# Kernel optimization log

Measured on AMD Instinct MI355X. Metric: run time of the kernel, lower is better.

The kernel has to match this reference:

```python
import jax, jax.numpy as jnp
import numpy as np

N_LEAVES = 32768
DEPTH = 16               # tree levels, leaves at level 0
N_NODES = 2 * N_LEAVES - 1
H = 256                  # h_size
X = 300                  # x_size
FEAT = 1024              # image feature_size
R = 49                   # image regions
VOCAB = 30000
CLASSES = 5


def setup_inputs() -> dict:
    ks = jax.random.split(jax.random.key(0), 10)
    wordid = jax.random.randint(ks[0], (N_NODES,), 0, VOCAB, dtype=jnp.int32)
    # leaves carry word tokens (mask=1), internal nodes don't (mask=0)
    mask = jnp.concatenate([jnp.ones(N_LEAVES, jnp.int32),
                            jnp.zeros(N_NODES - N_LEAVES, jnp.int32)])
    image = jax.random.normal(ks[1], (R, FEAT), dtype=jnp.float32)
    h0 = jnp.zeros((N_NODES, H), jnp.float32)
    c0 = jnp.zeros((N_NODES, H), jnp.float32)
    s = lambda k, shp, fan: jax.random.normal(k, shp, dtype=jnp.float32) * (1.0 / np.sqrt(fan))
    emb = s(ks[2], (VOCAB, X), X)
    attn_w_in = s(ks[3], (X, FEAT), FEAT)            # Attention.linear_in (no bias)
    attn_w_out = s(ks[4], (X, X + FEAT), X + FEAT)   # Attention.linear_out
    attn_b_out = jnp.zeros((X,), jnp.float32)
    w_iou = s(ks[5], (3 * H, X), X)                  # cell.W_iou (no bias)
    u_iou = s(ks[6], (3 * H, 2 * H), 2 * H)          # cell.U_iou (no bias)
    b_iou = jnp.zeros((1, 3 * H), jnp.float32)
    u_f_w = s(ks[7], (2 * H, 2 * H), 2 * H)          # cell.U_f
    u_f_b = jnp.zeros((2 * H,), jnp.float32)
    lin_w = s(ks[8], (CLASSES, H), H)                # final classifier
    lin_b = jnp.zeros((CLASSES,), jnp.float32)
    return dict(wordid=wordid, mask=mask, image=image, h0=h0, c0=c0, emb=emb,
                attn_w_in=attn_w_in, attn_w_out=attn_w_out, attn_b_out=attn_b_out,
                w_iou=w_iou, u_iou=u_iou, b_iou=b_iou, u_f_w=u_f_w, u_f_b=u_f_b,
                lin_w=lin_w, lin_b=lin_b)


def _forward(wordid, mask, image, h0, c0, emb, attn_w_in, attn_w_out, attn_b_out,
             w_iou, u_iou, b_iou, u_f_w, u_f_b, lin_w, lin_b):
    # --- embedding + attention over image regions ---
    embeds = emb[wordid * mask]                                  # [N, X]
    img_in = image @ attn_w_in.T                                 # [R, X]
    atten = jax.nn.softmax(embeds @ img_in.T, axis=1)            # [N, R]
    context = atten @ image                                      # [N, FEAT]
    sent = jnp.tanh(jnp.concatenate([context, embeds], axis=1) @ attn_w_out.T + attn_b_out)
    iou_x = (sent @ w_iou.T) * mask[:, None].astype(sent.dtype)  # [N, 3H] (dropout p=0 -> identity)

    def apply_node(iou, c_in):
        i, o, u = jnp.split(iou + b_iou, 3, axis=1)
        c_new = jax.nn.sigmoid(i) * jnp.tanh(u) + c_in
        return jax.nn.sigmoid(o) * jnp.tanh(c_new), c_new

    # --- leaves: no mailbox, apply_node with initial c ---
    h_leaf, c_leaf = apply_node(iou_x[:N_LEAVES], c0[:N_LEAVES])
    h = h0.at[:N_LEAVES].set(h_leaf)
    c = c0.at[:N_LEAVES].set(c_leaf)

    # --- topological propagation, one dense level at a time ---
    off_prev, sz, off = 0, N_LEAVES, N_LEAVES
    for _ in range(DEPTH - 1):
        sz_new = sz // 2
        h_cat = jax.lax.dynamic_slice_in_dim(h, off_prev, sz).reshape(sz_new, 2 * H)
        c_ch = jax.lax.dynamic_slice_in_dim(c, off_prev, sz).reshape(sz_new, 2, H)
        f = jax.nn.sigmoid(h_cat @ u_f_w.T + u_f_b).reshape(sz_new, 2, H)
        c_red = jnp.sum(f * c_ch, axis=1)                        # [sz_new, H]
        iou = h_cat @ u_iou.T                                    # reduce_func overwrites node iou
        h_new, c_new = apply_node(iou, c_red)
        h = h.at[off:off + sz_new].set(h_new)
        c = c.at[off:off + sz_new].set(c_new)
        off_prev, sz, off = off, sz_new, off + sz_new

    return h @ lin_w.T + lin_b                                   # [N, CLASSES]


def reference(wordid, mask, image, h0, c0, emb, attn_w_in, attn_w_out, attn_b_out,
              w_iou, u_iou, b_iou, u_f_w, u_f_b, lin_w, lin_b):
    return _forward(wordid, mask, image, h0, c0, emb, attn_w_in, attn_w_out, attn_b_out,
                    w_iou, u_iou, b_iou, u_f_w, u_f_b, lin_w, lin_b)
```

## Files before the change

kernel.cpp:

```cpp
#include <hip/hip_runtime.h>
#include <hip/hip_bf16.h>
#include <math.h>

#define N_LEAVES 32768
#define N_NODES  65535
#define DEPTH    16
#define H        256
#define XS       300
#define FEAT     1024
#define RR       49
#define CLASSES  5

#define XP 320
#define CATW 384

typedef __attribute__((ext_vector_type(8))) short bf16x8;
typedef __attribute__((ext_vector_type(4))) float f32x4;

__device__ __forceinline__ ushort f2bf(float v) {
    __hip_bfloat16 h = __float2bfloat16(v);
    return *reinterpret_cast<ushort*>(&h);
}
__device__ __forceinline__ float bf2f(ushort u) {
    __hip_bfloat16 h; *reinterpret_cast<ushort*>(&h) = u;
    return __bfloat162float(h);
}

__device__ __forceinline__ float fsig(float x) {
    float e = __builtin_amdgcn_exp2f(-1.44269504f * x);
    return __builtin_amdgcn_rcpf(1.0f + e);
}
__device__ __forceinline__ float ftanh(float x) {
    float xx = fmaxf(x, -20.0f);
    float e = __builtin_amdgcn_exp2f(-2.88539008f * xx);
    return (1.0f - e) * __builtin_amdgcn_rcpf(1.0f + e);
}
__device__ __forceinline__ float fexp(float x) {
    return __builtin_amdgcn_exp2f(1.44269504f * x);
}

#define SPIN() __builtin_amdgcn_sched_barrier(0)
#define SBAR() { __builtin_amdgcn_s_barrier(); __builtin_amdgcn_sched_barrier(0); }

__device__ __forceinline__ void swz_mj(int& mblk, int& jg) {
    int lid = blockIdx.y * gridDim.x + blockIdx.x;
    int mcount = gridDim.y, njg = gridDim.x;
    if ((mcount & 7) == 0) {
        int xcd = lid & 7, q = lid >> 3;
        jg = q % njg;
        mblk = xcd * (mcount >> 3) + q / njg;
    } else { mblk = blockIdx.y; jg = blockIdx.x; }
}

__device__ __forceinline__ ushort* lds_at(ushort* base, int row, int kbyte) {
    int off = row * 128 + kbyte;
    off ^= ((row & 7) << 4);
    return (ushort*)((char*)base + off);
}

__device__ __forceinline__ void gll16(const void* g, void* l) {
    __builtin_amdgcn_global_load_lds(
        (const __attribute__((address_space(1))) unsigned int*)g,
        (__attribute__((address_space(3))) unsigned int*)l, 16, 0, 0);
}

__device__ __forceinline__ void issue_tileA(const ushort* A, long lda, long m0, long mmax,
                                            int k0, ushort* buf, int R, int w, int lane)
{
    const int insts = R >> 5;
#pragma unroll
    for (int q = 0; q < 4; ++q) {
        if (q >= insts) break;
        int dest = (w * insts + q) * 1024;
        int row = (dest >> 7) + (lane >> 3);
        int kb = ((lane & 7) << 4) ^ ((row & 7) << 4);
        long am = m0 + row; if (am > mmax) am = mmax;
        gll16((const char*)(A + am * lda + k0) + kb, (char*)buf + dest);
    }
}

__global__ __launch_bounds__(256)
void k_sent(const ushort* __restrict__ A, const ushort* __restrict__ Wf,
            const float* __restrict__ bias, ushort* __restrict__ Cbf)
{
    __shared__ ushort At[3][128 * 64];
    const int tid = threadIdx.x;
    const int l = tid & 63;
    const int w = tid >> 6;
    int mblk, nb; swz_mj(mblk, nb);
    const long m0 = (long)mblk * 128;
    const ushort* wb = Wf + (size_t)(nb * 4 + w) * 24 * 512 + l * 8;

    bf16x8 wreg[2][2][2];
    f32x4 acc[2][8] = {};

    auto loadW = [&](int t, int buf) {
        const ushort* wt = wb + (long)t * 4 * 512;
#pragma unroll
        for (int kk = 0; kk < 2; ++kk)
#pragma unroll
            for (int j = 0; j < 2; ++j)
                wreg[buf][kk][j] = *(const bf16x8*)(wt + (long)(kk * 2 + j) * 512);
    };

    issue_tileA(A, CATW, m0, N_LEAVES - 1, 0, At[0], 128, w, l);
    __syncthreads();
    issue_tileA(A, CATW, m0, N_LEAVES - 1, 64, At[1], 128, w, l);
    SPIN();
    loadW(0, 0);
#pragma unroll
    for (int t = 0; t < 6; ++t) {
        if (t + 2 < 6) issue_tileA(A, CATW, m0, N_LEAVES - 1, (t + 2) * 64, At[(t + 2) % 3], 128, w, l);
        SPIN();
        if (t + 1 < 6) loadW(t + 1, (t + 1) & 1);
        ushort* Ab = At[t % 3];
#pragma unroll
        for (int kk = 0; kk < 2; ++kk) {
            bf16x8 af[8];
#pragma unroll
            for (int i = 0; i < 8; ++i)
                af[i] = *(const bf16x8*)lds_at(Ab, i * 16 + (l & 15), kk * 64 + (l >> 4) * 16);
#pragma unroll
            for (int j = 0; j < 2; ++j)
#pragma unroll
                for (int i = 0; i < 8; ++i)
                    acc[j][i] = __builtin_amdgcn_mfma_f32_16x16x32_bf16(af[i], wreg[t & 1][kk][j], acc[j][i], 0, 0, 0);
        }
        if (t + 1 < 6) SBAR();
    }
#pragma unroll
    for (int j = 0; j < 2; ++j) {
        long n = (long)nb * 128 + w * 32 + j * 16 + (l & 15);
        if (n >= XS) continue;
        float bn = bias[n];
#pragma unroll
        for (int i = 0; i < 8; ++i)
#pragma unroll
            for (int r = 0; r < 4; ++r) {
                long m = m0 + i * 16 + (l >> 4) * 4 + r;
                Cbf[m * XP + n] = f2bf(ftanh(acc[j][i][r] + bn));
            }
    }
}

__global__ __launch_bounds__(256)
void k_attn(const float* __restrict__ emb, const int* __restrict__ wid,
            const ushort* __restrict__ img, ushort* __restrict__ cat)
{
    __shared__ ushort At[128 * 64];
    __shared__ ushort Bt[64 * 64];
    const int tid = threadIdx.x;
    const int l = tid & 63;
    const int w = tid >> 6;
    const long m0 = (long)blockIdx.x * 128;
    const int srow = tid >> 3, skg = tid & 7;

    int wrd[4];
#pragma unroll
    for (int q = 0; q < 4; ++q) wrd[q] = wid[m0 + q * 32 + srow];

    float av[4][8];
    bf16x8 breg[2];
    f32x4 acc[2][4] = {};

    auto loadAB = [&](int t) {
        int c = t * 64 + skg * 8;
#pragma unroll
        for (int q = 0; q < 4; ++q) {
            const float* er = emb + (long)wrd[q] * XS;
            if (c + 8 <= XS) {
                float4 a = *(const float4*)(er + c);
                float4 b = *(const float4*)(er + c + 4);
                av[q][0] = a.x; av[q][1] = a.y; av[q][2] = a.z; av[q][3] = a.w;
                av[q][4] = b.x; av[q][5] = b.y; av[q][6] = b.z; av[q][7] = b.w;
            } else {
#pragma unroll
                for (int u = 0; u < 8; ++u) av[q][u] = (c + u < XS) ? er[c + u] : 0.f;
            }
        }
#pragma unroll
        for (int q = 0; q < 2; ++q)
            breg[q] = *(const bf16x8*)(img + (long)(q * 32 + srow) * XP + t * 64 + skg * 8);
    };
    auto writeAB = [&](int t) {
        int c = t * 64 + skg * 8;
#pragma unroll
        for (int q = 0; q < 4; ++q) {
            int row = q * 32 + srow;
            bf16x8 pk;
#pragma unroll
            for (int u = 0; u < 8; ++u) pk[u] = (short)f2bf(av[q][u]);
            *(bf16x8*)lds_at(At, row, skg * 16) = pk;
            *(bf16x8*)(cat + (m0 + row) * CATW + 64 + c) = pk;
        }
#pragma unroll
        for (int q = 0; q < 2; ++q)
            *(bf16x8*)lds_at(Bt, q * 32 + srow, skg * 16) = breg[q];
    };

    loadAB(0);
    writeAB(0);
    for (int t = 0; t < 5; ++t) {
        __syncthreads();
        if (t + 1 < 5) loadAB(t + 1);
#pragma unroll
        for (int kk = 0; kk < 2; ++kk) {
            bf16x8 af[2], bg[4];
#pragma unroll
            for (int i = 0; i < 2; ++i)
                af[i] = *(const bf16x8*)lds_at(At, w * 32 + i * 16 + (l & 15), kk * 64 + (l >> 4) * 16);
#pragma unroll
            for (int j = 0; j < 4; ++j)
                bg[j] = *(const bf16x8*)lds_at(Bt, j * 16 + (l & 15), kk * 64 + (l >> 4) * 16);
#pragma unroll
            for (int i = 0; i < 2; ++i)
#pragma unroll
                for (int j = 0; j < 4; ++j)
                    acc[i][j] = __builtin_amdgcn_mfma_f32_16x16x32_bf16(af[i], bg[j], acc[i][j], 0, 0, 0);
        }
        if (t + 1 < 5) {
            __syncthreads();
            writeAB(t + 1);
        }
    }
#pragma unroll
    for (int i = 0; i < 2; ++i)
#pragma unroll
        for (int r = 0; r < 4; ++r) {
            long m = m0 + w * 32 + i * 16 + (l >> 4) * 4 + r;
            float v[4]; float mx = -1e30f;
#pragma unroll
            for (int j = 0; j < 4; ++j) {
                int n = j * 16 + (l & 15);
                v[j] = (n < RR) ? acc[i][j][r] : -1e30f;
                mx = fmaxf(mx, v[j]);
            }
#pragma unroll
            for (int sh = 1; sh < 16; sh <<= 1) mx = fmaxf(mx, __shfl_xor(mx, sh));
            float e[4], s = 0.f;
#pragma unroll
            for (int j = 0; j < 4; ++j) { e[j] = fexp(v[j] - mx); s += e[j]; }
#pragma unroll
            for (int sh = 1; sh < 16; sh <<= 1) s += __shfl_xor(s, sh);
            float inv = __builtin_amdgcn_rcpf(s);
#pragma unroll
            for (int j = 0; j < 4; ++j)
                cat[m * CATW + j * 16 + (l & 15)] = f2bf(e[j] * inv);
        }
}

__global__ __launch_bounds__(256)
void k_leaf_fused(const ushort* __restrict__ A, const ushort* __restrict__ Wf,
                  const float* __restrict__ b_iou,
                  ushort* __restrict__ h, ushort* __restrict__ c)
{
    __shared__ ushort At[3][128 * 64];
    const int tid = threadIdx.x;
    const int l = tid & 63;
    const int w = tid >> 6;
    int mblk, jg; swz_mj(mblk, jg);
    const long m0 = (long)mblk * 128;
    const ushort* wb = Wf + (size_t)(jg * 4 + w) * 30 * 512 + l * 8;

    bf16x8 wreg[2][2][3];
    f32x4 acc[3][8] = {};

    auto loadW = [&](int t, int buf) {
        const ushort* wt = wb + (long)t * 6 * 512;
#pragma unroll
        for (int kk = 0; kk < 2; ++kk)
#pragma unroll
            for (int g = 0; g < 3; ++g)
                wreg[buf][kk][g] = *(const bf16x8*)(wt + (long)(kk * 3 + g) * 512);
    };

    issue_tileA(A, XP, m0, N_LEAVES - 1, 0, At[0], 128, w, l);
    __syncthreads();
    issue_tileA(A, XP, m0, N_LEAVES - 1, 64, At[1], 128, w, l);
    SPIN();
    loadW(0, 0);
#pragma unroll
    for (int t = 0; t < 5; ++t) {
        if (t + 2 < 5) issue_tileA(A, XP, m0, N_LEAVES - 1, (t + 2) * 64, At[(t + 2) % 3], 128, w, l);
        SPIN();
        if (t + 1 < 5) loadW(t + 1, (t + 1) & 1);
        ushort* Ab = At[t % 3];
#pragma unroll
        for (int kk = 0; kk < 2; ++kk) {
            bf16x8 af[8];
#pragma unroll
            for (int i = 0; i < 8; ++i)
                af[i] = *(const bf16x8*)lds_at(Ab, i * 16 + (l & 15), kk * 64 + (l >> 4) * 16);
#pragma unroll
            for (int g = 0; g < 3; ++g)
#pragma unroll
                for (int i = 0; i < 8; ++i)
                    acc[g][i] = __builtin_amdgcn_mfma_f32_16x16x32_bf16(af[i], wreg[t & 1][kk][g], acc[g][i], 0, 0, 0);
        }
        if (t + 1 < 5) SBAR();
    }
    {
        int jglob = jg * 64 + w * 16 + (l & 15);
        float bi = b_iou[jglob], bu = b_iou[512 + jglob], bo = b_iou[256 + jglob];
#pragma unroll
        for (int i = 0; i < 8; ++i)
#pragma unroll
            for (int r = 0; r < 4; ++r) {
                long m = m0 + i * 16 + (l >> 4) * 4 + r;
                float cn = fsig(acc[0][i][r] + bi) * ftanh(acc[1][i][r] + bu);
                c[m * H + jglob] = f2bf(cn);
                h[m * H + jglob] = f2bf(fsig(acc[2][i][r] + bo) * ftanh(cn));
            }
    }
}

__global__ __launch_bounds__(256)
void k_tree_fused(const ushort* __restrict__ A, const ushort* __restrict__ Wf,
                  const float* __restrict__ u_f_b, const float* __restrict__ b_iou,
                  const ushort* __restrict__ csrc,
                  ushort* __restrict__ hdst, ushort* __restrict__ cdst, int sz_new)
{
    __shared__ ushort At[3][64 * 64];
    const int tid = threadIdx.x;
    const int l = tid & 63;
    const int w = tid >> 6;
    int mblk, jg; swz_mj(mblk, jg);
    const long m0 = (long)mblk * 64;
    const ushort* wb = Wf + (size_t)(jg * 4 + w) * 80 * 512 + l * 8;

    bf16x8 wreg[2][2][5];
    f32x4 acc[5][4] = {};

    auto loadW = [&](int t, int buf) {
        const ushort* wt = wb + (long)t * 10 * 512;
#pragma unroll
        for (int kk = 0; kk < 2; ++kk)
#pragma unroll
            for (int g = 0; g < 5; ++g)
                wreg[buf][kk][g] = *(const bf16x8*)(wt + (long)(kk * 5 + g) * 512);
    };

    issue_tileA(A, 512, m0, sz_new - 1, 0, At[0], 64, w, l);
    __syncthreads();
    issue_tileA(A, 512, m0, sz_new - 1, 64, At[1], 64, w, l);
    SPIN();
    loadW(0, 0);
#pragma unroll
    for (int t = 0; t < 8; ++t) {
        if (t + 2 < 8) issue_tileA(A, 512, m0, sz_new - 1, (t + 2) * 64, At[(t + 2) % 3], 64, w, l);
        SPIN();
        if (t + 1 < 8) loadW(t + 1, (t + 1) & 1);
        ushort* Ab = At[t % 3];
#pragma unroll
        for (int kk = 0; kk < 2; ++kk) {
            bf16x8 af[4];
#pragma unroll
            for (int i = 0; i < 4; ++i)
                af[i] = *(const bf16x8*)lds_at(Ab, i * 16 + (l & 15), kk * 64 + (l >> 4) * 16);
#pragma unroll
            for (int g = 0; g < 5; ++g)
#pragma unroll
                for (int i = 0; i < 4; ++i)
                    acc[g][i] = __builtin_amdgcn_mfma_f32_16x16x32_bf16(af[i], wreg[t & 1][kk][g], acc[g][i], 0, 0, 0);
        }
        if (t + 1 < 8) SBAR();
    }
    {
        int jglob = jg * 64 + w * 16 + (l & 15);
        float bf0 = u_f_b[jglob], bf1 = u_f_b[256 + jglob];
        float bi = b_iou[jglob], bu = b_iou[512 + jglob], bo = b_iou[256 + jglob];
#pragma unroll
        for (int i = 0; i < 4; ++i)
#pragma unroll
            for (int r = 0; r < 4; ++r) {
                long m = m0 + i * 16 + (l >> 4) * 4 + r;
                if (m < sz_new) {
                    float cl = bf2f(csrc[(2 * m) * H + jglob]);
                    float cr = bf2f(csrc[(2 * m + 1) * H + jglob]);
                    float S = fsig(acc[0][i][r] + bf0) * cl
                            + fsig(acc[1][i][r] + bf1) * cr;
                    float cn = fsig(acc[2][i][r] + bi) * ftanh(acc[3][i][r] + bu) + S;
                    cdst[m * H + jglob] = f2bf(cn);
                    hdst[m * H + jglob] = f2bf(fsig(acc[4][i][r] + bo) * ftanh(cn));
                }
            }
    }
}

__global__ __launch_bounds__(256)
void k_prep(const float* __restrict__ image, const float* __restrict__ w_in,
            const float* __restrict__ w_out, ushort* __restrict__ img_bf,
            ushort* __restrict__ wcat)
{
    const int wave = (blockIdx.x * 256 + threadIdx.x) >> 6;
    const int lane = threadIdx.x & 63;
    const int half = RR * XS;
    if (wave >= 2 * half) return;
    const float* wr; const float* ir; ushort* outp;
    if (wave < half) {
        int r = wave / XS, x = wave % XS;
        ir = image + (long)r * FEAT;
        wr = w_in + (long)x * FEAT;
        outp = img_bf + (long)r * XP + x;
    } else {
        int w2 = wave - half;
        int x = w2 / RR, r = w2 % RR;
        ir = image + (long)r * FEAT;
        wr = w_out + (long)x * (FEAT + XS);
        outp = wcat + (long)x * CATW + r;
    }
    float s = 0.f;
#pragma unroll
    for (int u = 0; u < FEAT / 64; ++u) {
        int f = lane + u * 64;
        s = fmaf(ir[f], wr[f], s);
    }
#pragma unroll
    for (int sh = 32; sh; sh >>= 1) s += __shfl_xor(s, sh);
    if (lane == 0) *outp = f2bf(s);
}

__global__ __launch_bounds__(256)
void k_cvt(ushort* __restrict__ dst, long dld, long doff,
           const float* __restrict__ src, long sld, long soff,
           int rows, int cols)
{
    long idx = (long)blockIdx.x * 256 + threadIdx.x;
    if (idx >= (long)rows * cols) return;
    int r = (int)(idx / cols), c = (int)(idx % cols);
    dst[r * dld + doff + c] = f2bf(src[r * sld + soff + c]);
}

__global__ __launch_bounds__(256)
void k_bld_wcatf(ushort* __restrict__ dst, const ushort* __restrict__ wcat)
{
    long idx = (long)blockIdx.x * 256 + threadIdx.x;
    if (idx >= 147456) return;
    int u = idx & 7; long r = idx >> 3;
    int l = r & 63; r >>= 6;
    int j = r & 1; r >>= 1;
    int kk = r & 1; r >>= 1;
    int t = (int)(r % 6); r /= 6;
    int wq = r & 3; r >>= 2;
    int nb = (int)r;
    int row = nb * 128 + wq * 32 + j * 16 + (l & 15);
    int col = t * 64 + kk * 32 + (l >> 4) * 8 + u;
    dst[idx] = wcat[(long)row * CATW + col];
}

__global__ __launch_bounds__(256)
void k_bld_w3f(ushort* __restrict__ dst, const float* __restrict__ w_iou)
{
    long idx = (long)blockIdx.x * 256 + threadIdx.x;
    if (idx >= 245760) return;
    int u = idx & 7; long r = idx >> 3;
    int l = r & 63; r >>= 6;
    int g = (int)(r % 3); r /= 3;
    int kk = r & 1; r >>= 1;
    int t = (int)(r % 5); r /= 5;
    int wq = r & 3; r >>= 2;
    int jg = (int)r;
    int row = jg * 64 + wq * 16 + (l & 15);
    int col = t * 64 + kk * 32 + (l >> 4) * 8 + u;
    int srow = (g == 0) ? row : (g == 1) ? 512 + row : 256 + row;
    dst[idx] = (col < XS) ? f2bf(w_iou[(long)srow * XS + col]) : 0;
}

__global__ __launch_bounds__(256)
void k_bld_w5f(ushort* __restrict__ dst, const float* __restrict__ u_f_w,
               const float* __restrict__ u_iou)
{
    long idx = (long)blockIdx.x * 256 + threadIdx.x;
    if (idx >= 655360) return;
    int u = idx & 7; long r = idx >> 3;
    int l = r & 63; r >>= 6;
    int g = (int)(r % 5); r /= 5;
    int kk = r & 1; r >>= 1;
    int t = (int)(r & 7); r >>= 3;
    int wq = r & 3; r >>= 2;
    int jg = (int)r;
    int row = jg * 64 + wq * 16 + (l & 15);
    int col = t * 64 + kk * 32 + (l >> 4) * 8 + u;
    const float* src;
    if (g == 0)      src = u_f_w + (long)row * 512;
    else if (g == 1) src = u_f_w + (long)(256 + row) * 512;
    else if (g == 2) src = u_iou + (long)row * 512;
    else if (g == 3) src = u_iou + (long)(512 + row) * 512;
    else             src = u_iou + (long)(256 + row) * 512;
    dst[idx] = f2bf(src[col]);
}

__global__ __launch_bounds__(256)
void k_classify(const ushort* __restrict__ h, const float* __restrict__ lin_w,
                const float* __restrict__ lin_b, float* __restrict__ out, int n_rows)
{
    const int node = (int)((blockIdx.x * 256 + threadIdx.x) >> 6);
    const int lane = threadIdx.x & 63;
    if (node >= n_rows) return;
    const ushort* hr = h + (long)node * H;
    float p[CLASSES] = {0.f};
#pragma unroll
    for (int u = 0; u < H / 64; ++u) {
        int j = lane + u * 64;
        float hv = bf2f(hr[j]);
#pragma unroll
        for (int cc = 0; cc < CLASSES; ++cc)
            p[cc] = fmaf(hv, lin_w[cc * H + j], p[cc]);
    }
#pragma unroll
    for (int cc = 0; cc < CLASSES; ++cc)
#pragma unroll
        for (int sh = 32; sh; sh >>= 1) p[cc] += __shfl_xor(p[cc], sh);
    if (lane == 0) {
#pragma unroll
        for (int cc = 0; cc < CLASSES; ++cc)
            out[(long)node * CLASSES + cc] = p[cc] + lin_b[cc];
    }
}

extern "C" void kernel_launch(void* const* d_in, const int* in_sizes, int n_in,
                              void* d_out, int out_size, void* d_ws, size_t ws_size,
                              hipStream_t stream)
{
    const int*   wordid     = (const int*)  d_in[0];
    const float* image      = (const float*)d_in[2];
    const float* emb        = (const float*)d_in[5];
    const float* attn_w_in  = (const float*)d_in[6];
    const float* attn_w_out = (const float*)d_in[7];
    const float* attn_b_out = (const float*)d_in[8];
    const float* w_iou      = (const float*)d_in[9];
    const float* u_iou      = (const float*)d_in[10];
    const float* b_iou      = (const float*)d_in[11];
    const float* u_f_w      = (const float*)d_in[12];
    const float* u_f_b      = (const float*)d_in[13];
    const float* lin_w      = (const float*)d_in[14];
    const float* lin_b      = (const float*)d_in[15];
    float* out = (float*)d_out;

    char* p = (char*)d_ws;
    auto alloc = [&](size_t bytes) { char* r = p; p += (bytes + 255) & ~255UL; return r; };
    ushort* cat     = (ushort*)alloc((size_t)N_LEAVES * CATW * 2);
    ushort* sentbf  = (ushort*)alloc((size_t)N_LEAVES * XP * 2);
    ushort* hall    = (ushort*)alloc((size_t)65536 * H * 2);
    ushort* cA      = (ushort*)alloc((size_t)N_LEAVES * H * 2);
    ushort* cB      = (ushort*)alloc((size_t)(N_LEAVES/2) * H * 2);
    ushort* img_bf  = (ushort*)alloc((size_t)64 * XP * 2);
    ushort* wcat    = (ushort*)alloc((size_t)CATW * CATW * 2);
    ushort* wcatf   = (ushort*)alloc((size_t)147456 * 2);
    ushort* w3f     = (ushort*)alloc((size_t)245760 * 2);
    ushort* w5f     = (ushort*)alloc((size_t)655360 * 2);
    (void)ws_size;

    hipMemsetAsync(img_bf, 0, (size_t)64 * XP * 2, stream);
    hipMemsetAsync(wcat,   0, (size_t)CATW * CATW * 2, stream);
    {
        int waves = 2 * RR * XS;
        k_prep<<<(waves * 64 + 255) / 256, 256, 0, stream>>>(image, attn_w_in,
                                                             attn_w_out, img_bf, wcat);
    }
    k_cvt<<<((long)XS * XS + 255) / 256, 256, 0, stream>>>(
        wcat, CATW, 64, attn_w_out, FEAT + XS, FEAT, XS, XS);
    k_bld_wcatf<<<(147456 + 255) / 256, 256, 0, stream>>>(wcatf, wcat);
    k_bld_w3f<<<(245760 + 255) / 256, 256, 0, stream>>>(w3f, w_iou);
    k_bld_w5f<<<(655360 + 255) / 256, 256, 0, stream>>>(w5f, u_f_w, u_iou);

    k_attn<<<N_LEAVES / 128, 256, 0, stream>>>(emb, wordid, img_bf, cat);
    k_sent<<<dim3(3, N_LEAVES / 128), 256, 0, stream>>>(cat, wcatf, attn_b_out, sentbf);
    k_leaf_fused<<<dim3(4, N_LEAVES / 128), 256, 0, stream>>>(
        sentbf, w3f, b_iou, hall, cA);

    ushort* csrc = cA; ushort* cdst = cB;
    int node_off = N_LEAVES;
    int sz = N_LEAVES;
    int off_prev = 0;
    for (int lvl = 0; lvl < DEPTH - 1; ++lvl) {
        int sz_new = sz / 2;
        k_tree_fused<<<dim3(4, (sz_new + 63) / 64), 256, 0, stream>>>(
            hall + (long)off_prev * H, w5f, u_f_b, b_iou, csrc,
            hall + (long)node_off * H, cdst, sz_new);
        off_prev = node_off;
        node_off += sz_new;
        ushort* t = csrc; csrc = cdst; cdst = t;
        sz = sz_new;
    }

    k_classify<<<((long)N_NODES * 64 + 255) / 256, 256, 0, stream>>>(
        hall, lin_w, lin_b, out, N_NODES);
}
```

Before: 315.4 us.

## Deepen tree-kernel A-tile pipeline, merge prep kernels, vectorize classifier

The tree-level kernel now keeps four LDS A-tile buffers with a prefetch distance of three, and issues the next weight-register load before the wait rather than after. The four setup kernels (image projection, conversion, w3f and w5f builds) are merged into one launch that dispatches on block index, cutting launch overhead. The classifier now reads h and lin_w with vector loads. Risks include higher LDS use, which may lower occupancy, and an extra barrier per iteration in the tree kernel.

```diff
diff --git a/kernel.cpp b/kernel.cpp
--- a/kernel.cpp
+++ b/kernel.cpp
@@ -320,7 +320,7 @@
                   const ushort* __restrict__ csrc,
                   ushort* __restrict__ hdst, ushort* __restrict__ cdst, int sz_new)
 {
-    __shared__ ushort At[3][64 * 64];
+    __shared__ ushort At[4][64 * 64];
     const int tid = threadIdx.x;
     const int l = tid & 63;
     const int w = tid >> 6;
@@ -345,12 +345,15 @@
     issue_tileA(A, 512, m0, sz_new - 1, 64, At[1], 64, w, l);
     SPIN();
     loadW(0, 0);
+    SPIN();
+    issue_tileA(A, 512, m0, sz_new - 1, 128, At[2], 64, w, l);
 #pragma unroll
     for (int t = 0; t < 8; ++t) {
-        if (t + 2 < 8) issue_tileA(A, 512, m0, sz_new - 1, (t + 2) * 64, At[(t + 2) % 3], 64, w, l);
+        if (t + 1 < 8) loadW(t + 1, (t + 1) & 1);
         SPIN();
-        if (t + 1 < 8) loadW(t + 1, (t + 1) & 1);
-        ushort* Ab = At[t % 3];
+        if (t + 3 < 8) issue_tileA(A, 512, m0, sz_new - 1, (t + 3) * 64, At[(t + 3) & 3], 64, w, l);
+        SPIN();
+        ushort* Ab = At[t & 3];
 #pragma unroll
         for (int kk = 0; kk < 2; ++kk) {
             bf16x8 af[4];
@@ -387,52 +390,89 @@
     }
 }
 
-__global__ __launch_bounds__(256)
-void k_prep(const float* __restrict__ image, const float* __restrict__ w_in,
-            const float* __restrict__ w_out, ushort* __restrict__ img_bf,
-            ushort* __restrict__ wcat)
-{
-    const int wave = (blockIdx.x * 256 + threadIdx.x) >> 6;
-    const int lane = threadIdx.x & 63;
-    const int half = RR * XS;
-    if (wave >= 2 * half) return;
-    const float* wr; const float* ir; ushort* outp;
-    if (wave < half) {
-        int r = wave / XS, x = wave % XS;
-        ir = image + (long)r * FEAT;
-        wr = w_in + (long)x * FEAT;
-        outp = img_bf + (long)r * XP + x;
+#define PREP_NB   7350
+#define CVT_NB    352
+#define W3F_NB    960
+#define W5F_NB    2560
+
+__global__ __launch_bounds__(256)
+void k_prep_a(const float* __restrict__ image, const float* __restrict__ w_in,
+              const float* __restrict__ w_out, const float* __restrict__ w_iou,
+              const float* __restrict__ u_f_w, const float* __restrict__ u_iou,
+              ushort* __restrict__ img_bf, ushort* __restrict__ wcat,
+              ushort* __restrict__ w3f, ushort* __restrict__ w5f)
+{
+    int b = blockIdx.x;
+    if (b < PREP_NB) {
+        const int wave = (b * 256 + threadIdx.x) >> 6;
+        const int lane = threadIdx.x & 63;
+        const int half = RR * XS;
+        if (wave >= 2 * half) return;
+        const float* wr; const float* ir; ushort* outp;
+        if (wave < half) {
+            int r = wave / XS, x = wave % XS;
+            ir = image + (long)r * FEAT;
+            wr = w_in + (long)x * FEAT;
+            outp = img_bf + (long)r * XP + x;
+        } else {
+            int w2 = wave - half;
+            int x = w2 / RR, r = w2 % RR;
+            ir = image + (long)r * FEAT;
+            wr = w_out + (long)x * (FEAT + XS);
+            outp = wcat + (long)x * CATW + r;
+        }
+        float s = 0.f;
+#pragma unroll
+        for (int u = 0; u < FEAT / 64; ++u) {
+            int f = lane + u * 64;
+            s = fmaf(ir[f], wr[f], s);
+        }
+#pragma unroll
+        for (int sh = 32; sh; sh >>= 1) s += __shfl_xor(s, sh);
+        if (lane == 0) *outp = f2bf(s);
+    } else if (b < PREP_NB + CVT_NB) {
+        long idx = (long)(b - PREP_NB) * 256 + threadIdx.x;
+        if (idx >= (long)XS * XS) return;
+        int r = (int)(idx / XS), cc = (int)(idx % XS);
+        wcat[(long)r * CATW + 64 + cc] = f2bf(w_out[(long)r * (FEAT + XS) + FEAT + cc]);
+    } else if (b < PREP_NB + CVT_NB + W3F_NB) {
+        long idx = (long)(b - PREP_NB - CVT_NB) * 256 + threadIdx.x;
+        if (idx >= 245760) return;
+        int u = idx & 7; long r = idx >> 3;
+        int l = r & 63; r >>= 6;
+        int g = (int)(r % 3); r /= 3;
+        int kk = r & 1; r >>= 1;
+        int t = (int)(r % 5); r /= 5;
+        int wq = r & 3; r >>= 2;
+        int jg = (int)r;
+        int row = jg * 64 + wq * 16 + (l & 15);
+        int col = t * 64 + kk * 32 + (l >> 4) * 8 + u;
+        int srow = (g == 0) ? row : (g == 1) ? 512 + row : 256 + row;
+        w3f[idx] = (col < XS) ? f2bf(w_iou[(long)srow * XS + col]) : 0;
     } else {
-        int w2 = wave - half;
-        int x = w2 / RR, r = w2 % RR;
-        ir = image + (long)r * FEAT;
-        wr = w_out + (long)x * (FEAT + XS);
-        outp = wcat + (long)x * CATW + r;
-    }
-    float s = 0.f;
-#pragma unroll
-    for (int u = 0; u < FEAT / 64; ++u) {
-        int f = lane + u * 64;
-        s = fmaf(ir[f], wr[f], s);
-    }
-#pragma unroll
-    for (int sh = 32; sh; sh >>= 1) s += __shfl_xor(s, sh);
-    if (lane == 0) *outp = f2bf(s);
-}
-
-__global__ __launch_bounds__(256)
-void k_cvt(ushort* __restrict__ dst, long dld, long doff,
-           const float* __restrict__ src, long sld, long soff,
-           int rows, int cols)
-{
-    long idx = (long)blockIdx.x * 256 + threadIdx.x;
-    if (idx >= (long)rows * cols) return;
-    int r = (int)(idx / cols), c = (int)(idx % cols);
-    dst[r * dld + doff + c] = f2bf(src[r * sld + soff + c]);
-}
-
-__global__ __launch_bounds__(256)
-void k_bld_wcatf(ushort* __restrict__ dst, const ushort* __restrict__ wcat)
+        long idx = (long)(b - PREP_NB - CVT_NB - W3F_NB) * 256 + threadIdx.x;
+        if (idx >= 655360) return;
+        int u = idx & 7; long r = idx >> 3;
+        int l = r & 63; r >>= 6;
+        int g = (int)(r % 5); r /= 5;
+        int kk = r & 1; r >>= 1;
+        int t = (int)(r & 7); r >>= 3;
+        int wq = r & 3; r >>= 2;
+        int jg = (int)r;
+        int row = jg * 64 + wq * 16 + (l & 15);
+        int col = t * 64 + kk * 32 + (l >> 4) * 8 + u;
+        const float* src;
+        if (g == 0)      src = u_f_w + (long)row * 512;
+        else if (g == 1) src = u_f_w + (long)(256 + row) * 512;
+        else if (g == 2) src = u_iou + (long)row * 512;
+        else if (g == 3) src = u_iou + (long)(512 + row) * 512;
+        else             src = u_iou + (long)(256 + row) * 512;
+        w5f[idx] = f2bf(src[col]);
+    }
+}
+
+__global__ __launch_bounds__(256)
+void k_prep_b(ushort* __restrict__ dst, const ushort* __restrict__ wcat)
 {
     long idx = (long)blockIdx.x * 256 + threadIdx.x;
     if (idx >= 147456) return;
@@ -449,63 +489,19 @@
 }
 
 __global__ __launch_bounds__(256)
-void k_bld_w3f(ushort* __restrict__ dst, const float* __restrict__ w_iou)
-{
-    long idx = (long)blockIdx.x * 256 + threadIdx.x;
-    if (idx >= 245760) return;
-    int u = idx & 7; long r = idx >> 3;
-    int l = r & 63; r >>= 6;
-    int g = (int)(r % 3); r /= 3;
-    int kk = r & 1; r >>= 1;
-    int t = (int)(r % 5); r /= 5;
-    int wq = r & 3; r >>= 2;
-    int jg = (int)r;
-    int row = jg * 64 + wq * 16 + (l & 15);
-    int col = t * 64 + kk * 32 + (l >> 4) * 8 + u;
-    int srow = (g == 0) ? row : (g == 1) ? 512 + row : 256 + row;
-    dst[idx] = (col < XS) ? f2bf(w_iou[(long)srow * XS + col]) : 0;
-}
-
-__global__ __launch_bounds__(256)
-void k_bld_w5f(ushort* __restrict__ dst, const float* __restrict__ u_f_w,
-               const float* __restrict__ u_iou)
-{
-    long idx = (long)blockIdx.x * 256 + threadIdx.x;
-    if (idx >= 655360) return;
-    int u = idx & 7; long r = idx >> 3;
-    int l = r & 63; r >>= 6;
-    int g = (int)(r % 5); r /= 5;
-    int kk = r & 1; r >>= 1;
-    int t = (int)(r & 7); r >>= 3;
-    int wq = r & 3; r >>= 2;
-    int jg = (int)r;
-    int row = jg * 64 + wq * 16 + (l & 15);
-    int col = t * 64 + kk * 32 + (l >> 4) * 8 + u;
-    const float* src;
-    if (g == 0)      src = u_f_w + (long)row * 512;
-    else if (g == 1) src = u_f_w + (long)(256 + row) * 512;
-    else if (g == 2) src = u_iou + (long)row * 512;
-    else if (g == 3) src = u_iou + (long)(512 + row) * 512;
-    else             src = u_iou + (long)(256 + row) * 512;
-    dst[idx] = f2bf(src[col]);
-}
-
-__global__ __launch_bounds__(256)
 void k_classify(const ushort* __restrict__ h, const float* __restrict__ lin_w,
                 const float* __restrict__ lin_b, float* __restrict__ out, int n_rows)
 {
     const int node = (int)((blockIdx.x * 256 + threadIdx.x) >> 6);
     const int lane = threadIdx.x & 63;
     if (node >= n_rows) return;
-    const ushort* hr = h + (long)node * H;
-    float p[CLASSES] = {0.f};
-#pragma unroll
-    for (int u = 0; u < H / 64; ++u) {
-        int j = lane + u * 64;
-        float hv = bf2f(hr[j]);
-#pragma unroll
-        for (int cc = 0; cc < CLASSES; ++cc)
-            p[cc] = fmaf(hv, lin_w[cc * H + j], p[cc]);
+    ushort4 hv4 = *(const ushort4*)(h + (long)node * H + lane * 4);
+    float hv[4] = { bf2f(hv4.x), bf2f(hv4.y), bf2f(hv4.z), bf2f(hv4.w) };
+    float p[CLASSES];
+#pragma unroll
+    for (int cc = 0; cc < CLASSES; ++cc) {
+        float4 wv = *(const float4*)(lin_w + (long)cc * H + lane * 4);
+        p[cc] = hv[0] * wv.x + hv[1] * wv.y + hv[2] * wv.z + hv[3] * wv.w;
     }
 #pragma unroll
     for (int cc = 0; cc < CLASSES; ++cc)
@@ -553,16 +549,10 @@
 
     hipMemsetAsync(img_bf, 0, (size_t)64 * XP * 2, stream);
     hipMemsetAsync(wcat,   0, (size_t)CATW * CATW * 2, stream);
-    {
-        int waves = 2 * RR * XS;
-        k_prep<<<(waves * 64 + 255) / 256, 256, 0, stream>>>(image, attn_w_in,
-                                                             attn_w_out, img_bf, wcat);
-    }
-    k_cvt<<<((long)XS * XS + 255) / 256, 256, 0, stream>>>(
-        wcat, CATW, 64, attn_w_out, FEAT + XS, FEAT, XS, XS);
-    k_bld_wcatf<<<(147456 + 255) / 256, 256, 0, stream>>>(wcatf, wcat);
-    k_bld_w3f<<<(245760 + 255) / 256, 256, 0, stream>>>(w3f, w_iou);
-    k_bld_w5f<<<(655360 + 255) / 256, 256, 0, stream>>>(w5f, u_f_w, u_iou);
+    k_prep_a<<<PREP_NB + CVT_NB + W3F_NB + W5F_NB, 256, 0, stream>>>(
+        image, attn_w_in, attn_w_out, w_iou, u_f_w, u_iou,
+        img_bf, wcat, w3f, w5f);
+    k_prep_b<<<(147456 + 255) / 256, 256, 0, stream>>>(wcatf, wcat);
 
     k_attn<<<N_LEAVES / 128, 256, 0, stream>>>(emb, wordid, img_bf, cat);
     k_sent<<<dim3(3, N_LEAVES / 128), 256, 0, stream>>>(cat, wcatf, attn_b_out, sentbf);
```

New measurement: 311.6 us. No clear change (-1.2%).
